# Optimization experiments

Measured on AMD Instinct MI355X. Metric: run time of the kernel, lower is better.

Reference implementation:

```python
import jax, jax.numpy as jnp
import numpy as np

H = 32   # hidden_dim
L = 2    # rnn_num_layers
T = 52   # num_steps / seq_len
F = 64   # n_features (== 2*H, so layer-1 input size matches layer-0)
B = 8192 # batch


def _cell(x, h, c, Wih, Whh, b):
    # PyTorch LSTM gate order: i, f, g, o. b = b_ih + b_hh (mathematically identical).
    g = x @ Wih.T + h @ Whh.T + b
    i, f, gg, o = jnp.split(g, 4, axis=-1)
    c2 = jax.nn.sigmoid(f) * c + jax.nn.sigmoid(i) * jnp.tanh(gg)
    h2 = jax.nn.sigmoid(o) * jnp.tanh(c2)
    return h2, c2


def _encoder(x, h0, c0, Wih, Whh, b):
    # x: [B,T,F]; h0/c0: [2L,B,H]; PyTorch stacking order: [l0_fwd, l0_bwd, l1_fwd, l1_bwd]
    xs = jnp.swapaxes(x, 0, 1)  # time-major [T,B,F]
    hn, cn = [], []
    for l in range(L):
        def step_fwd(carry, xt):
            h, c = carry
            h2, c2 = _cell(xt, h, c, Wih[l, 0], Whh[l, 0], b[l, 0])
            return (h2, c2), h2
        def step_bwd(carry, xt):
            h, c = carry
            h2, c2 = _cell(xt, h, c, Wih[l, 1], Whh[l, 1], b[l, 1])
            return (h2, c2), h2
        (hf, cf), of = jax.lax.scan(step_fwd, (h0[2 * l], c0[2 * l]), xs)
        (hb, cb), ob = jax.lax.scan(step_bwd, (h0[2 * l + 1], c0[2 * l + 1]), xs[::-1])
        xs = jnp.concatenate([of, ob[::-1]], axis=-1)  # [T,B,2H]
        hn += [hf, hb]
        cn += [cf, cb]
    hn = jnp.stack(hn)  # [4,B,H]
    cn = jnp.stack(cn)
    hc = jnp.concatenate([jnp.swapaxes(hn, 0, 1), jnp.swapaxes(cn, 0, 1)], axis=1)  # [B,8,H]
    return hc.reshape(hc.shape[0], -1)  # [B, 2*2L*H] = [B,256]


def _decoder(code, Wih, Whh, b):
    Bn = code.shape[0]
    _code = code.reshape(Bn, 2, 2 * L, H)       # [B, (h,c), 4, H]
    h = jnp.swapaxes(_code[:, 0], 0, 1)          # [4,B,H]
    c = jnp.swapaxes(_code[:, 1], 0, 1)
    out0 = jnp.zeros((Bn, F), code.dtype)

    def step(carry, _):
        out, h, c = carry
        y = out
        hs, cs = [], []
        for l in range(L):
            hf, cf = _cell(y, h[2 * l], c[2 * l], Wih[l, 0], Whh[l, 0], b[l, 0])
            hb, cb = _cell(y, h[2 * l + 1], c[2 * l + 1], Wih[l, 1], Whh[l, 1], b[l, 1])
            y = jnp.concatenate([hf, hb], axis=-1)  # [B,2H]
            hs += [hf, hb]
            cs += [cf, cb]
        return (jax.lax.stop_gradient(y), jnp.stack(hs), jnp.stack(cs)), y

    _, ys = jax.lax.scan(step, (out0, h, c), None, length=T)  # ys: [T,B,F]
    return jnp.swapaxes(ys, 0, 1)  # [B,T,F]


def setup_inputs() -> dict:
    key = jax.random.key(0)
    ks = jax.random.split(key, 9)
    s = 1.0 / np.sqrt(H)  # PyTorch LSTM init range
    u = lambda k, shape: jax.random.uniform(k, shape, jnp.float32, -s, s)
    return {
        "x": jax.random.normal(ks[0], (B, T, F), jnp.float32),
        "h0": jax.random.normal(ks[1], (2 * L, B, H), jnp.float32),
        "c0": jax.random.normal(ks[2], (2 * L, B, H), jnp.float32),
        "enc_Wih": u(ks[3], (L, 2, 4 * H, F)),
        "enc_Whh": u(ks[4], (L, 2, 4 * H, H)),
        "enc_b": u(ks[5], (L, 2, 4 * H)),
        "dec_Wih": u(ks[6], (L, 2, 4 * H, F)),
        "dec_Whh": u(ks[7], (L, 2, 4 * H, H)),
        "dec_b": u(ks[8], (L, 2, 4 * H)),
    }


def reference(x, h0, c0, enc_Wih, enc_Whh, enc_b, dec_Wih, dec_Whh, dec_b):
    z = _encoder(x, h0, c0, enc_Wih, enc_Whh, enc_b)          # [B,256]
    x_hat = _decoder(z, dec_Wih, dec_Whh, dec_b)              # [B,T,F]
    return (x_hat, z)
```

## Files before the change

### kernel.cpp

```cpp
#include <hip/hip_runtime.h>
#include <cstddef>
#include <cstdint>

#define Tn 52
#define Fn 64
#define Hn 32
#define Bn 8192
#define XHAT_ELEMS (Bn * Tn * Fn)
#define L2E 1.44269504088896340736f

typedef __attribute__((ext_vector_type(8))) short bf8v;
typedef __attribute__((ext_vector_type(4))) float f4v;

__device__ __forceinline__ f4v mfma_bf16(bf8v a, bf8v b, f4v c) {
    return __builtin_amdgcn_mfma_f32_16x16x32_bf16(a, b, c, 0, 0, 0);
}

__device__ __forceinline__ void split_tr(float v, unsigned short& hi, unsigned short& lo) {
    unsigned b = __float_as_uint(v);
    hi = (unsigned short)(b >> 16);
    float lf = v - __uint_as_float(b & 0xFFFF0000u);
    lo = (unsigned short)(__float_as_uint(lf) >> 16);
}

__device__ __forceinline__ void split8v(float4 a, float4 b, bf8v& h, bf8v& l) {
    float v[8] = {a.x, a.y, a.z, a.w, b.x, b.y, b.z, b.w};
#pragma unroll
    for (int j = 0; j < 8; ++j) {
        unsigned bb = __float_as_uint(v[j]);
        h[j] = (short)(bb >> 16);
        float lf = v[j] - __uint_as_float(bb & 0xFFFF0000u);
        l[j] = (short)(__float_as_uint(lf) >> 16);
    }
}

__device__ __forceinline__ unsigned short rne_bf16(float v) {
    unsigned b = __float_as_uint(v);
    unsigned r = ((b >> 16) & 1u) + 0x7FFFu;
    return (unsigned short)((b + r) >> 16);
}

__device__ __forceinline__ void lds_barrier() {
    __builtin_amdgcn_sched_barrier(0);
    asm volatile("s_waitcnt lgkmcnt(0)" ::: "memory");
    __builtin_amdgcn_s_barrier();
    __builtin_amdgcn_sched_barrier(0);
}

__device__ __forceinline__ float lstm_one(float aI, float aF, float aG, float aO, float& cst) {
    float ei = exp2f(fminf(40.f, -aI));
    float ef = exp2f(fminf(40.f, -aF));
    float eg = exp2f(fminf(40.f, -aG));
    float eo = exp2f(fminf(40.f, -aO));
    float p   = (1.f + ei) * (1.f + eg);
    float num = cst * p + (1.f - eg) * (1.f + ef);
    float den = (1.f + ef) * p;
    float c2  = num * __builtin_amdgcn_rcpf(den);
    cst = c2;
    float e2 = exp2f(fminf(40.f, -2.f * L2E * c2));
    return (1.f - e2) * __builtin_amdgcn_rcpf((1.f + eo) * (1.f + e2));
}

#define GM2(ACC, AH, AL, WHx)        \
    ACC = mfma_bf16(AL, WHx, ACC);   \
    ACC = mfma_bf16(AH, WHx, ACC);

#define PINW(W)                                                               \
    asm volatile("" : "+v"(W[0][0]), "+v"(W[0][1]), "+v"(W[0][2]),            \
                      "+v"(W[1][0]), "+v"(W[1][1]), "+v"(W[1][2]));           \
    asm volatile("" : "+v"(W[2][0]), "+v"(W[2][1]), "+v"(W[2][2]),            \
                      "+v"(W[3][0]), "+v"(W[3][1]), "+v"(W[3][2]));

__global__ void prep_kernel(const float* __restrict__ eWih, const float* __restrict__ eWhh,
                            const float* __restrict__ dWih, const float* __restrict__ dWhh,
                            unsigned short* __restrict__ ws)
{
    int fid = blockIdx.x * 256 + threadIdx.x;
    if (fid >= 12288) return;
    int lane = fid & 63;
    int ki   = (fid >> 6) % 3;
    int nt   = (fid / 192) & 7;
    int cell = (fid / 1536) & 3;
    int grp  = fid / 6144;
    const float* Wih = grp ? dWih : eWih;
    const float* Whh = grp ? dWhh : eWhh;
    int gate = nt * 16 + (lane & 15);
    float scale = ((gate >> 5) == 2) ? 2.f * L2E : L2E;
    int k0 = ki * 32 + (lane >> 4) * 8;
    size_t base = (size_t)grp * 98304 + (size_t)cell * 12288 + nt * 1536 + ki * 512 + lane * 8;
#pragma unroll
    for (int j = 0; j < 8; ++j) {
        int k = k0 + j;
        float v = (k < 64) ? Wih[(size_t)cell * 8192 + gate * 64 + k]
                           : Whh[(size_t)cell * 4096 + gate * 32 + (k - 64)];
        ws[base + j] = rne_bf16(v * scale);
    }
}

template<int IS_L0>
__global__ __launch_bounds__(256, 2)
void enc_kernel(const float* __restrict__ X,
                const unsigned short* __restrict__ Xh, const unsigned short* __restrict__ Xl,
                const float* __restrict__ h0, const float* __restrict__ c0,
                const unsigned short* __restrict__ Whi, const float* __restrict__ bias,
                int layer,
                unsigned short* __restrict__ outh, unsigned short* __restrict__ outl,
                float* __restrict__ z)
{
    __shared__ __align__(16) unsigned short Hsh[2][2][16][40], Hsl[2][2][16][40];
    const int tid = threadIdx.x, w = tid >> 6, lane = tid & 63;
    const int d = w >> 1, q = w & 1;
    const int a = lane & 15, kb = lane >> 4;
    const int u = q * 16 + a;
    const int row0 = blockIdx.x * 16;
    const int ci = 2 * layer + d;

    bf8v WH[4][3];
#pragma unroll
    for (int g = 0; g < 4; ++g)
#pragma unroll
        for (int ki = 0; ki < 3; ++ki)
            WH[g][ki] = *(const bf8v*)(Whi + (size_t)ci * 12288 + (2 * g + q) * 1536
                                       + ki * 512 + lane * 8);
    float bj[4];
#pragma unroll
    for (int g = 0; g < 4; ++g)
        bj[g] = bias[ci * 128 + g * 32 + u] * ((g == 2) ? 2.f * L2E : L2E);
    float cst[4], hfin[4];
#pragma unroll
    for (int j = 0; j < 4; ++j)
        cst[j] = c0[((size_t)ci * Bn + row0 + 4 * kb + j) * Hn + u];

    {
        int dd = tid >> 7, rr = (tid >> 3) & 15, u4 = (tid & 7) * 4;
        const float* src = h0 + ((size_t)(2 * layer + dd) * Bn + row0 + rr) * Hn + u4;
#pragma unroll
        for (int e = 0; e < 4; ++e)
            split_tr(src[e], Hsh[dd][1][rr][u4 + e], Hsl[dd][1][rr][u4 + e]);
    }
    __syncthreads();

    const int grow = row0 + a;
    float4 p0, p1, p2, p3; bf8v ph0, pl0, ph1, pl1;
    {
        int tt = d ? (Tn - 1) : 0;
        if (IS_L0) {
            const float* sp = X + ((size_t)grow * Tn + tt) * Fn;
            p0 = *(const float4*)(sp + kb * 8);      p1 = *(const float4*)(sp + kb * 8 + 4);
            p2 = *(const float4*)(sp + 32 + kb * 8); p3 = *(const float4*)(sp + 32 + kb * 8 + 4);
        } else {
            size_t so = ((size_t)tt * Bn + grow) * Fn + kb * 8;
            ph0 = *(const bf8v*)(Xh + so);      pl0 = *(const bf8v*)(Xl + so);
            ph1 = *(const bf8v*)(Xh + so + 32); pl1 = *(const bf8v*)(Xl + so + 32);
        }
    }

    for (int t = 0; t < Tn; ++t) {
        PINW(WH);
        bf8v xh0, xl0, xh1, xl1;
        if (IS_L0) { split8v(p0, p1, xh0, xl0); split8v(p2, p3, xh1, xl1); }
        else       { xh0 = ph0; xl0 = pl0; xh1 = ph1; xl1 = pl1; }
        {
            int tn = (t + 1 < Tn) ? t + 1 : t;
            int tt = d ? (Tn - 1 - tn) : tn;
            if (IS_L0) {
                const float* sp = X + ((size_t)grow * Tn + tt) * Fn;
                p0 = *(const float4*)(sp + kb * 8);      p1 = *(const float4*)(sp + kb * 8 + 4);
                p2 = *(const float4*)(sp + 32 + kb * 8); p3 = *(const float4*)(sp + 32 + kb * 8 + 4);
            } else {
                size_t so = ((size_t)tt * Bn + grow) * Fn + kb * 8;
                ph0 = *(const bf8v*)(Xh + so);      pl0 = *(const bf8v*)(Xl + so);
                ph1 = *(const bf8v*)(Xh + so + 32); pl1 = *(const bf8v*)(Xl + so + 32);
            }
        }
        bf8v hh = *(const bf8v*)&Hsh[d][(t & 1) ^ 1][a][kb * 8];
        bf8v hl = *(const bf8v*)&Hsl[d][(t & 1) ^ 1][a][kb * 8];
        f4v acc[4];
#pragma unroll
        for (int g = 0; g < 4; ++g) acc[g] = (f4v){bj[g], bj[g], bj[g], bj[g]};
#pragma unroll
        for (int g = 0; g < 4; ++g) { GM2(acc[g], xh0, xl0, WH[g][0]); }
#pragma unroll
        for (int g = 0; g < 4; ++g) { GM2(acc[g], xh1, xl1, WH[g][1]); }
#pragma unroll
        for (int g = 0; g < 4; ++g) { GM2(acc[g], hh, hl, WH[g][2]); }
        int tp = d ? (Tn - 1 - t) : t;
#pragma unroll
        for (int j = 0; j < 4; ++j) {
            float hv = lstm_one(acc[0][j], acc[1][j], acc[2][j], acc[3][j], cst[j]);
            hfin[j] = hv;
            unsigned short hi_, lo_;
            split_tr(hv, hi_, lo_);
            Hsh[d][t & 1][4 * kb + j][u] = hi_;
            Hsl[d][t & 1][4 * kb + j][u] = lo_;
            if (IS_L0) {
                size_t o = ((size_t)tp * Bn + row0 + 4 * kb + j) * Fn + d * 32 + u;
                outh[o] = hi_;
                outl[o] = lo_;
            }
        }
        lds_barrier();
    }
#pragma unroll
    for (int j = 0; j < 4; ++j) {
        size_t zr = (size_t)(row0 + 4 * kb + j) * 256;
        z[zr + ci * 32 + u]       = hfin[j];
        z[zr + 128 + ci * 32 + u] = cst[j];
    }
}

__global__ __launch_bounds__(512, 2)
void dec_kernel(const unsigned short* __restrict__ Whi, const float* __restrict__ bias,
                const float* __restrict__ z, float* __restrict__ xhat)
{
    __shared__ __align__(16) unsigned short Ysh[2][2][16][72], Ysl[2][2][16][72];
    __shared__ __align__(16) unsigned short Msh[2][16][72],    Msl[2][16][72];
    __shared__ __align__(16) unsigned short Hsh[4][2][2][16][40], Hsl[4][2][2][16][40];

    const int tid = threadIdx.x, w = tid >> 6, lane = tid & 63;
    const int P = w >> 2, cl = (w >> 1) & 1, q = w & 1;
    const int cell = P * 2 + cl;
    const int a = lane & 15, kb = lane >> 4, u = q * 16 + a;
    const int row0 = blockIdx.x * 32;

    bf8v WH[4][3];
#pragma unroll
    for (int g = 0; g < 4; ++g)
#pragma unroll
        for (int ki = 0; ki < 3; ++ki)
            WH[g][ki] = *(const bf8v*)(Whi + (size_t)cell * 12288 + (2 * g + q) * 1536
                                       + ki * 512 + lane * 8);
    float bj[4];
#pragma unroll
    for (int g = 0; g < 4; ++g)
        bj[g] = bias[cell * 128 + g * 32 + u] * ((g == 2) ? 2.f * L2E : L2E);

    float cst[2][4];
#pragma unroll
    for (int G = 0; G < 2; ++G)
#pragma unroll
        for (int j = 0; j < 4; ++j)
            cst[G][j] = z[(size_t)(row0 + G * 16 + 4 * kb + j) * 256 + 128 + cell * 32 + u];

    {
        int ct = tid >> 7, rem = tid & 127, rr = rem >> 2, u8 = (rem & 3) * 8;
        const float* src = z + (size_t)(row0 + rr) * 256 + ct * 32 + u8;
#pragma unroll
        for (int e = 0; e < 8; ++e)
            split_tr(src[e], Hsh[ct][rr >> 4][1][rr & 15][u8 + e],
                             Hsl[ct][rr >> 4][1][rr & 15][u8 + e]);
    }
    for (int i = tid; i < 2 * 16 * 72; i += 512) {
        int G = (i >= 16 * 72) ? 1 : 0, rI = i - G * (16 * 72);
        Ysh[G][1][rI / 72][rI % 72] = 0;
        Ysl[G][1][rI / 72][rI % 72] = 0;
    }
    __syncthreads();

    auto cellstep = [&](int G, int t, bool isA) {
        const int par = t & 1, rpar = par ^ 1;
        f4v acc[4];
#pragma unroll
        for (int g = 0; g < 4; ++g) acc[g] = (f4v){bj[g], bj[g], bj[g], bj[g]};
        if (!isA || t > 0) {
            const unsigned short (*Vh)[72] = isA ? Ysh[G][rpar] : Msh[G];
            const unsigned short (*Vl)[72] = isA ? Ysl[G][rpar] : Msl[G];
            bf8v vh0 = *(const bf8v*)&Vh[a][kb * 8];
            bf8v vl0 = *(const bf8v*)&Vl[a][kb * 8];
            bf8v vh1 = *(const bf8v*)&Vh[a][32 + kb * 8];
            bf8v vl1 = *(const bf8v*)&Vl[a][32 + kb * 8];
#pragma unroll
            for (int g = 0; g < 4; ++g) { GM2(acc[g], vh0, vl0, WH[g][0]); }
#pragma unroll
            for (int g = 0; g < 4; ++g) { GM2(acc[g], vh1, vl1, WH[g][1]); }
        }
        bf8v hh = *(const bf8v*)&Hsh[cell][G][rpar][a][kb * 8];
        bf8v hl = *(const bf8v*)&Hsl[cell][G][rpar][a][kb * 8];
#pragma unroll
        for (int g = 0; g < 4; ++g) { GM2(acc[g], hh, hl, WH[g][2]); }
#pragma unroll
        for (int j = 0; j < 4; ++j) {
            float hv = lstm_one(acc[0][j], acc[1][j], acc[2][j], acc[3][j], cst[G][j]);
            unsigned short hi_, lo_;
            split_tr(hv, hi_, lo_);
            int r = 4 * kb + j;
            Hsh[cell][G][par][r][u] = hi_;
            Hsl[cell][G][par][r][u] = lo_;
            if (isA) {
                Msh[G][r][cl * 32 + u] = hi_;
                Msl[G][r][cl * 32 + u] = lo_;
            } else {
                Ysh[G][par][r][cl * 32 + u] = hi_;
                Ysl[G][par][r][cl * 32 + u] = lo_;
                xhat[((size_t)(row0 + G * 16 + r) * Tn + t) * Fn + cl * 32 + u] = hv;
            }
        }
    };

    for (int t = 0; t < Tn; ++t) {
        PINW(WH);
        if (P == 0)      cellstep(0, t, true);
        else if (t > 0)  cellstep(1, t - 1, false);
        lds_barrier();
        if (P == 0)      cellstep(1, t, true);
        else             cellstep(0, t, false);
        lds_barrier();
    }
    if (P == 1) cellstep(1, Tn - 1, false);
}

extern "C" void kernel_launch(void* const* d_in, const int* in_sizes, int n_in,
                              void* d_out, int out_size, void* d_ws, size_t ws_size,
                              hipStream_t stream) {
    const float* x    = (const float*)d_in[0];
    const float* h0   = (const float*)d_in[1];
    const float* c0   = (const float*)d_in[2];
    const float* eWih = (const float*)d_in[3];
    const float* eWhh = (const float*)d_in[4];
    const float* eb   = (const float*)d_in[5];
    const float* dWih = (const float*)d_in[6];
    const float* dWhh = (const float*)d_in[7];
    const float* db   = (const float*)d_in[8];

    float* out = (float*)d_out;
    unsigned short* xs1h = (unsigned short*)d_out;
    unsigned short* xs1l = xs1h + (size_t)XHAT_ELEMS;
    float* zb = out + (size_t)XHAT_ELEMS;
    unsigned short* wsb = (unsigned short*)d_ws;

    hipLaunchKernelGGL(prep_kernel, dim3(48), dim3(256), 0, stream,
                       eWih, eWhh, dWih, dWhh, wsb);
    hipLaunchKernelGGL((enc_kernel<1>), dim3(Bn / 16), dim3(256), 0, stream,
                       x, (const unsigned short*)nullptr, (const unsigned short*)nullptr,
                       h0, c0, wsb, eb, 0, xs1h, xs1l, zb);
    hipLaunchKernelGGL((enc_kernel<0>), dim3(Bn / 16), dim3(256), 0, stream,
                       (const float*)nullptr, xs1h, xs1l,
                       h0, c0, wsb, eb, 1,
                       (unsigned short*)nullptr, (unsigned short*)nullptr, zb);
    hipLaunchKernelGGL(dec_kernel, dim3(Bn / 32), dim3(512), 0, stream,
                       wsb + 98304, db, zb, out);
}
```

Before: 316.6 us.

## Drop split-bf16 hi/lo operands and hoist input projections off the recurrence path

Activations and hidden states were split into hi/lo bf16 pairs, so every GEMM fragment ran two MFMAs. They are now rounded once to bf16, which halves MFMA count, LDS traffic and the inter-layer activation buffer. The encoder and decoder loops are also restructured so the input-projection (or hidden-projection) MFMAs for the next step are issued before the barrier, keeping only one MFMA group on the serial dependency chain. The cost is lower precision, so accumulated recurrence error over 52 steps may exceed tolerance.

Result: faster. 267.6 us (-15.5%).

```diff
diff --git a/kernel.cpp b/kernel.cpp
--- a/kernel.cpp
+++ b/kernel.cpp
@@ -16,28 +16,18 @@
     return __builtin_amdgcn_mfma_f32_16x16x32_bf16(a, b, c, 0, 0, 0);
 }
 
-__device__ __forceinline__ void split_tr(float v, unsigned short& hi, unsigned short& lo) {
-    unsigned b = __float_as_uint(v);
-    hi = (unsigned short)(b >> 16);
-    float lf = v - __uint_as_float(b & 0xFFFF0000u);
-    lo = (unsigned short)(__float_as_uint(lf) >> 16);
-}
-
-__device__ __forceinline__ void split8v(float4 a, float4 b, bf8v& h, bf8v& l) {
-    float v[8] = {a.x, a.y, a.z, a.w, b.x, b.y, b.z, b.w};
-#pragma unroll
-    for (int j = 0; j < 8; ++j) {
-        unsigned bb = __float_as_uint(v[j]);
-        h[j] = (short)(bb >> 16);
-        float lf = v[j] - __uint_as_float(bb & 0xFFFF0000u);
-        l[j] = (short)(__float_as_uint(lf) >> 16);
-    }
-}
-
 __device__ __forceinline__ unsigned short rne_bf16(float v) {
     unsigned b = __float_as_uint(v);
     unsigned r = ((b >> 16) & 1u) + 0x7FFFu;
     return (unsigned short)((b + r) >> 16);
+}
+
+__device__ __forceinline__ bf8v rne8(float4 a, float4 b) {
+    float v[8] = {a.x, a.y, a.z, a.w, b.x, b.y, b.z, b.w};
+    bf8v r;
+#pragma unroll
+    for (int j = 0; j < 8; ++j) r[j] = (short)rne_bf16(v[j]);
+    return r;
 }
 
 __device__ __forceinline__ void lds_barrier() {
@@ -60,10 +50,6 @@
     float e2 = exp2f(fminf(40.f, -2.f * L2E * c2));
     return (1.f - e2) * __builtin_amdgcn_rcpf((1.f + eo) * (1.f + e2));
 }
-
-#define GM2(ACC, AH, AL, WHx)        \
-    ACC = mfma_bf16(AL, WHx, ACC);   \
-    ACC = mfma_bf16(AH, WHx, ACC);
 
 #define PINW(W)                                                               \
     asm volatile("" : "+v"(W[0][0]), "+v"(W[0][1]), "+v"(W[0][2]),            \
@@ -99,15 +85,12 @@
 
 template<int IS_L0>
 __global__ __launch_bounds__(256, 2)
-void enc_kernel(const float* __restrict__ X,
-                const unsigned short* __restrict__ Xh, const unsigned short* __restrict__ Xl,
+void enc_kernel(const float* __restrict__ X, const unsigned short* __restrict__ Xh,
                 const float* __restrict__ h0, const float* __restrict__ c0,
                 const unsigned short* __restrict__ Whi, const float* __restrict__ bias,
-                int layer,
-                unsigned short* __restrict__ outh, unsigned short* __restrict__ outl,
-                float* __restrict__ z)
+                int layer, unsigned short* __restrict__ outh, float* __restrict__ z)
 {
-    __shared__ __align__(16) unsigned short Hsh[2][2][16][40], Hsl[2][2][16][40];
+    __shared__ __align__(16) unsigned short Hsh[2][2][16][40];
     const int tid = threadIdx.x, w = tid >> 6, lane = tid & 63;
     const int d = w >> 1, q = w & 1;
     const int a = lane & 15, kb = lane >> 4;
@@ -136,67 +119,78 @@
         const float* src = h0 + ((size_t)(2 * layer + dd) * Bn + row0 + rr) * Hn + u4;
 #pragma unroll
         for (int e = 0; e < 4; ++e)
-            split_tr(src[e], Hsh[dd][1][rr][u4 + e], Hsl[dd][1][rr][u4 + e]);
+            Hsh[dd][1][rr][u4 + e] = rne_bf16(src[e]);
     }
     __syncthreads();
 
     const int grow = row0 + a;
-    float4 p0, p1, p2, p3; bf8v ph0, pl0, ph1, pl1;
+    float4 p0, p1, p2, p3; bf8v ph0, ph1;
+    f4v acc[4];
     {
         int tt = d ? (Tn - 1) : 0;
+        bf8v xf0, xf1;
         if (IS_L0) {
             const float* sp = X + ((size_t)grow * Tn + tt) * Fn;
+            xf0 = rne8(*(const float4*)(sp + kb * 8), *(const float4*)(sp + kb * 8 + 4));
+            xf1 = rne8(*(const float4*)(sp + 32 + kb * 8), *(const float4*)(sp + 32 + kb * 8 + 4));
+        } else {
+            size_t so = ((size_t)tt * Bn + grow) * Fn + kb * 8;
+            xf0 = *(const bf8v*)(Xh + so);
+            xf1 = *(const bf8v*)(Xh + so + 32);
+        }
+#pragma unroll
+        for (int g = 0; g < 4; ++g) {
+            acc[g] = (f4v){bj[g], bj[g], bj[g], bj[g]};
+            acc[g] = mfma_bf16(xf0, WH[g][0], acc[g]);
+            acc[g] = mfma_bf16(xf1, WH[g][1], acc[g]);
+        }
+        int tt1 = d ? (Tn - 2) : 1;
+        if (IS_L0) {
+            const float* sp = X + ((size_t)grow * Tn + tt1) * Fn;
             p0 = *(const float4*)(sp + kb * 8);      p1 = *(const float4*)(sp + kb * 8 + 4);
             p2 = *(const float4*)(sp + 32 + kb * 8); p3 = *(const float4*)(sp + 32 + kb * 8 + 4);
         } else {
-            size_t so = ((size_t)tt * Bn + grow) * Fn + kb * 8;
-            ph0 = *(const bf8v*)(Xh + so);      pl0 = *(const bf8v*)(Xl + so);
-            ph1 = *(const bf8v*)(Xh + so + 32); pl1 = *(const bf8v*)(Xl + so + 32);
+            size_t so = ((size_t)tt1 * Bn + grow) * Fn + kb * 8;
+            ph0 = *(const bf8v*)(Xh + so);
+            ph1 = *(const bf8v*)(Xh + so + 32);
         }
     }
 
     for (int t = 0; t < Tn; ++t) {
         PINW(WH);
-        bf8v xh0, xl0, xh1, xl1;
-        if (IS_L0) { split8v(p0, p1, xh0, xl0); split8v(p2, p3, xh1, xl1); }
-        else       { xh0 = ph0; xl0 = pl0; xh1 = ph1; xl1 = pl1; }
+        bf8v hh = *(const bf8v*)&Hsh[d][(t & 1) ^ 1][a][kb * 8];
+#pragma unroll
+        for (int g = 0; g < 4; ++g) acc[g] = mfma_bf16(hh, WH[g][2], acc[g]);
+        int tp = d ? (Tn - 1 - t) : t;
+#pragma unroll
+        for (int j = 0; j < 4; ++j) {
+            float hv = lstm_one(acc[0][j], acc[1][j], acc[2][j], acc[3][j], cst[j]);
+            hfin[j] = hv;
+            unsigned short hp = rne_bf16(hv);
+            Hsh[d][t & 1][4 * kb + j][u] = hp;
+            if (IS_L0)
+                outh[((size_t)tp * Bn + row0 + 4 * kb + j) * Fn + d * 32 + u] = hp;
+        }
         {
-            int tn = (t + 1 < Tn) ? t + 1 : t;
-            int tt = d ? (Tn - 1 - tn) : tn;
+            bf8v xf0, xf1;
+            if (IS_L0) { xf0 = rne8(p0, p1); xf1 = rne8(p2, p3); }
+            else       { xf0 = ph0; xf1 = ph1; }
+#pragma unroll
+            for (int g = 0; g < 4; ++g) {
+                f4v t0 = (f4v){bj[g], bj[g], bj[g], bj[g]};
+                t0 = mfma_bf16(xf0, WH[g][0], t0);
+                acc[g] = mfma_bf16(xf1, WH[g][1], t0);
+            }
+            int ts = (t + 2 < Tn) ? t + 2 : Tn - 1;
+            int tt = d ? (Tn - 1 - ts) : ts;
             if (IS_L0) {
                 const float* sp = X + ((size_t)grow * Tn + tt) * Fn;
                 p0 = *(const float4*)(sp + kb * 8);      p1 = *(const float4*)(sp + kb * 8 + 4);
                 p2 = *(const float4*)(sp + 32 + kb * 8); p3 = *(const float4*)(sp + 32 + kb * 8 + 4);
             } else {
                 size_t so = ((size_t)tt * Bn + grow) * Fn + kb * 8;
-                ph0 = *(const bf8v*)(Xh + so);      pl0 = *(const bf8v*)(Xl + so);
-                ph1 = *(const bf8v*)(Xh + so + 32); pl1 = *(const bf8v*)(Xl + so + 32);
-            }
-        }
-        bf8v hh = *(const bf8v*)&Hsh[d][(t & 1) ^ 1][a][kb * 8];
-        bf8v hl = *(const bf8v*)&Hsl[d][(t & 1) ^ 1][a][kb * 8];
-        f4v acc[4];
-#pragma unroll
-        for (int g = 0; g < 4; ++g) acc[g] = (f4v){bj[g], bj[g], bj[g], bj[g]};
-#pragma unroll
-        for (int g = 0; g < 4; ++g) { GM2(acc[g], xh0, xl0, WH[g][0]); }
-#pragma unroll
-        for (int g = 0; g < 4; ++g) { GM2(acc[g], xh1, xl1, WH[g][1]); }
-#pragma unroll
-        for (int g = 0; g < 4; ++g) { GM2(acc[g], hh, hl, WH[g][2]); }
-        int tp = d ? (Tn - 1 - t) : t;
-#pragma unroll
-        for (int j = 0; j < 4; ++j) {
-            float hv = lstm_one(acc[0][j], acc[1][j], acc[2][j], acc[3][j], cst[j]);
-            hfin[j] = hv;
-            unsigned short hi_, lo_;
-            split_tr(hv, hi_, lo_);
-            Hsh[d][t & 1][4 * kb + j][u] = hi_;
-            Hsl[d][t & 1][4 * kb + j][u] = lo_;
-            if (IS_L0) {
-                size_t o = ((size_t)tp * Bn + row0 + 4 * kb + j) * Fn + d * 32 + u;
-                outh[o] = hi_;
-                outl[o] = lo_;
+                ph0 = *(const bf8v*)(Xh + so);
+                ph1 = *(const bf8v*)(Xh + so + 32);
             }
         }
         lds_barrier();
@@ -213,9 +207,9 @@
 void dec_kernel(const unsigned short* __restrict__ Whi, const float* __restrict__ bias,
                 const float* __restrict__ z, float* __restrict__ xhat)
 {
-    __shared__ __align__(16) unsigned short Ysh[2][2][16][72], Ysl[2][2][16][72];
-    __shared__ __align__(16) unsigned short Msh[2][16][72],    Msl[2][16][72];
-    __shared__ __align__(16) unsigned short Hsh[4][2][2][16][40], Hsl[4][2][2][16][40];
+    __shared__ __align__(16) unsigned short Ysh[2][2][16][72];
+    __shared__ __align__(16) unsigned short Msh[2][16][72];
+    __shared__ __align__(16) unsigned short Hsh[4][2][2][16][40];
 
     const int tid = threadIdx.x, w = tid >> 6, lane = tid & 63;
     const int P = w >> 2, cl = (w >> 1) & 1, q = w & 1;
@@ -247,66 +241,56 @@
         const float* src = z + (size_t)(row0 + rr) * 256 + ct * 32 + u8;
 #pragma unroll
         for (int e = 0; e < 8; ++e)
-            split_tr(src[e], Hsh[ct][rr >> 4][1][rr & 15][u8 + e],
-                             Hsl[ct][rr >> 4][1][rr & 15][u8 + e]);
-    }
-    for (int i = tid; i < 2 * 16 * 72; i += 512) {
-        int G = (i >= 16 * 72) ? 1 : 0, rI = i - G * (16 * 72);
-        Ysh[G][1][rI / 72][rI % 72] = 0;
-        Ysl[G][1][rI / 72][rI % 72] = 0;
+            Hsh[ct][rr >> 4][1][rr & 15][u8 + e] = rne_bf16(src[e]);
     }
     __syncthreads();
 
-    auto cellstep = [&](int G, int t, bool isA) {
-        const int par = t & 1, rpar = par ^ 1;
-        f4v acc[4];
-#pragma unroll
-        for (int g = 0; g < 4; ++g) acc[g] = (f4v){bj[g], bj[g], bj[g], bj[g]};
-        if (!isA || t > 0) {
-            const unsigned short (*Vh)[72] = isA ? Ysh[G][rpar] : Msh[G];
-            const unsigned short (*Vl)[72] = isA ? Ysl[G][rpar] : Msl[G];
+    f4v accp[4];
+    auto hpart = [&](int G, int rpar) {
+        bf8v hh = *(const bf8v*)&Hsh[cell][G][rpar][a][kb * 8];
+#pragma unroll
+        for (int g = 0; g < 4; ++g) {
+            f4v t0 = (f4v){bj[g], bj[g], bj[g], bj[g]};
+            accp[g] = mfma_bf16(hh, WH[g][2], t0);
+        }
+    };
+    auto finish = [&](int G, int t, bool isA, bool hasV) {
+        if (hasV) {
+            const unsigned short (*Vh)[72] = isA ? Ysh[G][(t - 1) & 1] : Msh[G];
             bf8v vh0 = *(const bf8v*)&Vh[a][kb * 8];
-            bf8v vl0 = *(const bf8v*)&Vl[a][kb * 8];
             bf8v vh1 = *(const bf8v*)&Vh[a][32 + kb * 8];
-            bf8v vl1 = *(const bf8v*)&Vl[a][32 + kb * 8];
-#pragma unroll
-            for (int g = 0; g < 4; ++g) { GM2(acc[g], vh0, vl0, WH[g][0]); }
-#pragma unroll
-            for (int g = 0; g < 4; ++g) { GM2(acc[g], vh1, vl1, WH[g][1]); }
-        }
-        bf8v hh = *(const bf8v*)&Hsh[cell][G][rpar][a][kb * 8];
-        bf8v hl = *(const bf8v*)&Hsl[cell][G][rpar][a][kb * 8];
-#pragma unroll
-        for (int g = 0; g < 4; ++g) { GM2(acc[g], hh, hl, WH[g][2]); }
+#pragma unroll
+            for (int g = 0; g < 4; ++g) {
+                accp[g] = mfma_bf16(vh0, WH[g][0], accp[g]);
+                accp[g] = mfma_bf16(vh1, WH[g][1], accp[g]);
+            }
+        }
 #pragma unroll
         for (int j = 0; j < 4; ++j) {
-            float hv = lstm_one(acc[0][j], acc[1][j], acc[2][j], acc[3][j], cst[G][j]);
-            unsigned short hi_, lo_;
-            split_tr(hv, hi_, lo_);
+            float hv = lstm_one(accp[0][j], accp[1][j], accp[2][j], accp[3][j], cst[G][j]);
+            unsigned short hp = rne_bf16(hv);
             int r = 4 * kb + j;
-            Hsh[cell][G][par][r][u] = hi_;
-            Hsl[cell][G][par][r][u] = lo_;
+            Hsh[cell][G][t & 1][r][u] = hp;
             if (isA) {
-                Msh[G][r][cl * 32 + u] = hi_;
-                Msl[G][r][cl * 32 + u] = lo_;
+                Msh[G][r][cl * 32 + u] = hp;
             } else {
-                Ysh[G][par][r][cl * 32 + u] = hi_;
-                Ysl[G][par][r][cl * 32 + u] = lo_;
+                Ysh[G][t & 1][r][cl * 32 + u] = hp;
                 xhat[((size_t)(row0 + G * 16 + r) * Tn + t) * Fn + cl * 32 + u] = hv;
             }
         }
     };
 
+    hpart(0, 1);
     for (int t = 0; t < Tn; ++t) {
         PINW(WH);
-        if (P == 0)      cellstep(0, t, true);
-        else if (t > 0)  cellstep(1, t - 1, false);
+        if (P == 0) { finish(0, t, true, t > 0);       hpart(1, (t - 1) & 1); }
+        else        { if (t > 0) finish(1, t - 1, false, true); hpart(0, (t - 1) & 1); }
         lds_barrier();
-        if (P == 0)      cellstep(1, t, true);
-        else             cellstep(0, t, false);
+        if (P == 0) { finish(1, t, true, t > 0);       hpart(0, t & 1); }
+        else        { finish(0, t, false, true);       hpart(1, (t & 1) ^ 1); }
         lds_barrier();
     }
-    if (P == 1) cellstep(1, Tn - 1, false);
+    if (P == 1) finish(1, Tn - 1, false, true);
 }
 
 extern "C" void kernel_launch(void* const* d_in, const int* in_sizes, int n_in,
@@ -324,19 +308,17 @@
 
     float* out = (float*)d_out;
     unsigned short* xs1h = (unsigned short*)d_out;
-    unsigned short* xs1l = xs1h + (size_t)XHAT_ELEMS;
     float* zb = out + (size_t)XHAT_ELEMS;
     unsigned short* wsb = (unsigned short*)d_ws;
 
     hipLaunchKernelGGL(prep_kernel, dim3(48), dim3(256), 0, stream,
                        eWih, eWhh, dWih, dWhh, wsb);
     hipLaunchKernelGGL((enc_kernel<1>), dim3(Bn / 16), dim3(256), 0, stream,
-                       x, (const unsigned short*)nullptr, (const unsigned short*)nullptr,
-                       h0, c0, wsb, eb, 0, xs1h, xs1l, zb);
+                       x, (const unsigned short*)nullptr,
+                       h0, c0, wsb, eb, 0, xs1h, zb);
     hipLaunchKernelGGL((enc_kernel<0>), dim3(Bn / 16), dim3(256), 0, stream,
-                       (const float*)nullptr, xs1h, xs1l,
-                       h0, c0, wsb, eb, 1,
-                       (unsigned short*)nullptr, (unsigned short*)nullptr, zb);
+                       (const float*)nullptr, xs1h,
+                       h0, c0, wsb, eb, 1, (unsigned short*)nullptr, zb);
     hipLaunchKernelGGL(dec_kernel, dim3(Bn / 32), dim3(512), 0, stream,
                        wsb + 98304, db, zb, out);
 }
```
